# Kernel tuning notes

Measured on AMD Instinct MI355X. Metric: run time of the kernel, lower is better.

## Reference

```python
import jax, jax.numpy as jnp
import numpy as np

HIDDEN = 1024
HEADS = 16
D_K = HIDDEN // HEADS
NEG_INF = -jnp.inf


def setup_inputs() -> dict:
    key = jax.random.key(0)
    ks = jax.random.split(key, 9)
    N, S = 4, 2048
    scale = 1.0 / np.sqrt(HIDDEN)
    x = jax.random.normal(ks[0], (N, S, HIDDEN), dtype=jnp.float32)
    attn_mask = jnp.ones((N, S), dtype=jnp.int32)
    Wq = jax.random.normal(ks[1], (HIDDEN, HIDDEN), dtype=jnp.float32) * scale
    bq = jnp.zeros((HIDDEN,), dtype=jnp.float32)
    Wk = jax.random.normal(ks[2], (HIDDEN, HIDDEN), dtype=jnp.float32) * scale
    bk = jnp.zeros((HIDDEN,), dtype=jnp.float32)
    Wv = jax.random.normal(ks[3], (HIDDEN, HIDDEN), dtype=jnp.float32) * scale
    bv = jnp.zeros((HIDDEN,), dtype=jnp.float32)
    Wp = jax.random.normal(ks[4], (HIDDEN, HIDDEN), dtype=jnp.float32) * scale
    bp = jnp.zeros((HIDDEN,), dtype=jnp.float32)
    return {"x": x, "attn_mask": attn_mask, "Wq": Wq, "bq": bq,
            "Wk": Wk, "bk": bk, "Wv": Wv, "bv": bv, "Wp": Wp, "bp": bp}


def reference(x, attn_mask, Wq, bq, Wk, bk, Wv, bv, Wp, bp):
    N, S, _ = x.shape
    H, dk = HEADS, D_K
    # torch nn.Linear: y = x @ W.T + b
    q = (x @ Wq.T + bq).reshape(N, S, H, dk).transpose(0, 2, 1, 3)  # (N,H,S,dk)
    k = (x @ Wk.T + bk).reshape(N, S, H, dk).transpose(0, 2, 1, 3)
    v = (x @ Wv.T + bv).reshape(N, S, H, dk).transpose(0, 2, 1, 3)
    attn = jnp.einsum('nhqd,nhkd->nhqk', q, k) / jnp.sqrt(jnp.float32(dk))
    mask = attn_mask.reshape(N, 1, 1, S)
    attn = jnp.where(mask == 0, NEG_INF, attn)
    attn = jax.nn.softmax(attn, axis=-1)
    # dropout is identity in eval mode
    y = jnp.einsum('nhqk,nhkd->nhqd', attn, v)  # (N,H,S,dk)
    y = y.transpose(0, 2, 1, 3).reshape(N, S, H * dk)
    return y @ Wp.T + bp
```

## Files before the change

kernel.cpp:

```cpp
#include <hip/hip_runtime.h>

typedef unsigned short u16;
typedef unsigned int u32;
typedef unsigned long long u64;
typedef __attribute__((ext_vector_type(8))) short bf16x8;
typedef __attribute__((ext_vector_type(4))) short bf16x4;
typedef __attribute__((ext_vector_type(4))) float f32x4;
typedef __attribute__((ext_vector_type(2))) unsigned int u32x2;

#define AS1(p) ((const __attribute__((address_space(1))) void*)(p))
#define AS3(p) ((__attribute__((address_space(3))) void*)(p))

__device__ __forceinline__ u16 f2bf(float f) {
    u32 u = __float_as_uint(f);
    u += 0x7fff + ((u >> 16) & 1);
    return (u16)(u >> 16);
}
__device__ __forceinline__ u32 pack2bf(float lo, float hi) {
    u32 a = __float_as_uint(lo) + 0x8000u;
    u32 b = __float_as_uint(hi) + 0x8000u;
    return __builtin_amdgcn_perm(b, a, 0x07060302);
}
__device__ __forceinline__ u32 cvtpk(float lo, float hi) {
    u32 r;
    asm("v_cvt_pk_bf16_f32 %0, %1, %2" : "=v"(r) : "v"(lo), "v"(hi));
    return r;
}

__device__ __forceinline__ void async16(const u16* g, u16* l) {
    __builtin_amdgcn_global_load_lds(AS1(g), AS3(l), 16, 0, 0);
}

__global__ __launch_bounds__(256) void cvt_kernel(const float* __restrict__ src,
                                                  u16* __restrict__ dst, int n) {
    int idx = (blockIdx.x * 256 + threadIdx.x) * 8;
    if (idx >= n) return;
    float4 a = *(const float4*)(src + idx);
    float4 b = *(const float4*)(src + idx + 4);
    uint4 o;
    o.x = (u32)f2bf(a.x) | ((u32)f2bf(a.y) << 16);
    o.y = (u32)f2bf(a.z) | ((u32)f2bf(a.w) << 16);
    o.z = (u32)f2bf(b.x) | ((u32)f2bf(b.y) << 16);
    o.w = (u32)f2bf(b.z) | ((u32)f2bf(b.w) << 16);
    *(uint4*)(dst + idx) = o;
}

__global__ __launch_bounds__(256) void cvt4_kernel(
    const float* __restrict__ s0, const float* __restrict__ s1,
    const float* __restrict__ s2, const float* __restrict__ s3,
    u16* __restrict__ d0, u16* __restrict__ d1,
    u16* __restrict__ d2, u16* __restrict__ d3) {
    const float* s; u16* d;
    switch (blockIdx.y) {
        case 0:  s = s0; d = d0; break;
        case 1:  s = s1; d = d1; break;
        case 2:  s = s2; d = d2; break;
        default: s = s3; d = d3; break;
    }
    int idx = (blockIdx.x * 256 + threadIdx.x) * 8;
    float4 a = *(const float4*)(s + idx);
    float4 b = *(const float4*)(s + idx + 4);
    uint4 o;
    o.x = (u32)f2bf(a.x) | ((u32)f2bf(a.y) << 16);
    o.y = (u32)f2bf(a.z) | ((u32)f2bf(a.w) << 16);
    o.z = (u32)f2bf(b.x) | ((u32)f2bf(b.y) << 16);
    o.w = (u32)f2bf(b.z) | ((u32)f2bf(b.w) << 16);
    *(uint4*)(d + idx) = o;
}

__global__ __launch_bounds__(256, 2) void gemm_bt(
    const u16* __restrict__ A,
    const u16* __restrict__ Wa, const u16* __restrict__ Wb, const u16* __restrict__ Wc,
    const float* __restrict__ ba, const float* __restrict__ bb, const float* __restrict__ bc,
    void* oa, void* ob_, void* oc, int mode)
{
    constexpr int K = 1024;
    __shared__ u16 smem[128 * 132];

    const int tid = threadIdx.x;
    const int lane = tid & 63, wv = tid >> 6;
    const int l15 = lane & 15, quad = lane >> 4;
    const int wr = wv >> 1, wc = wv & 1;

    const int L = blockIdx.x + (blockIdx.y << 3) + (blockIdx.z << 9);
    const int g = L & 7;
    const int j = L >> 3;
    const int z = j >> 6;
    const int r = j & 63;
    const int m0 = ((g << 3) + (r & 7)) * 128;
    const int n0 = (r >> 3) * 128;

    const u16* W = (z == 0) ? Wa : ((z == 1) ? Wb : Wc);
    const float* bs = (z == 0) ? ba : ((z == 1) ? bb : bc);
    void* out = (z == 0) ? oa : ((z == 1) ? ob_ : oc);
    const bool swap_ = (mode == 1) || (z < 2);

    f32x4 acc[4][4];
#pragma unroll
    for (int i = 0; i < 4; ++i)
#pragma unroll
        for (int j2 = 0; j2 < 4; ++j2) acc[i][j2] = (f32x4)0.f;

    const int c0 = (wv * 2) * 64 + lane;
    const int c1 = c0 + 64;
    const int row0 = c0 >> 2, row1 = c1 >> 2;
    const int ko0 = ((c0 & 3) ^ (row0 & 3)) * 8;
    const int ko1 = ((c1 & 3) ^ (row1 & 3)) * 8;
    const u16* As0 = A + (size_t)(m0 + row0) * K + ko0;
    const u16* As1 = A + (size_t)(m0 + row1) * K + ko1;
    const u16* Ws0 = W + (size_t)(n0 + row0) * K + ko0;
    const u16* Ws1 = W + (size_t)(n0 + row1) * K + ko1;
    const int off0 = c0 * 8, off1 = c1 * 8;

    u16* const At0 = smem;         u16* const Wt0 = smem + 4096;
    u16* const At1 = smem + 8192;  u16* const Wt1 = smem + 12288;

    auto stage = [&](u16* Atb, u16* Wtb, int kk) {
        async16(As0 + kk, Atb + off0);
        async16(As1 + kk, Atb + off1);
        async16(Ws0 + kk, Wtb + off0);
        async16(Ws1 + kk, Wtb + off1);
    };
    auto compute = [&](const u16* Atb, const u16* Wtb) {
        bf16x8 af[4], wf[4];
#pragma unroll
        for (int t = 0; t < 4; ++t) {
            int rowa = wr * 64 + t * 16 + l15;
            af[t] = *(const bf16x8*)&Atb[rowa * 32 + ((quad ^ (rowa & 3)) * 8)];
            int rowb = wc * 64 + t * 16 + l15;
            wf[t] = *(const bf16x8*)&Wtb[rowb * 32 + ((quad ^ (rowb & 3)) * 8)];
        }
        if (swap_) {
#pragma unroll
            for (int rt = 0; rt < 4; ++rt)
#pragma unroll
                for (int ct = 0; ct < 4; ++ct)
                    acc[rt][ct] = __builtin_amdgcn_mfma_f32_16x16x32_bf16(wf[ct], af[rt], acc[rt][ct], 0, 0, 0);
        } else {
#pragma unroll
            for (int rt = 0; rt < 4; ++rt)
#pragma unroll
                for (int ct = 0; ct < 4; ++ct)
                    acc[rt][ct] = __builtin_amdgcn_mfma_f32_16x16x32_bf16(af[rt], wf[ct], acc[rt][ct], 0, 0, 0);
        }
    };

    stage(At0, Wt0, 0);
    asm volatile("s_waitcnt vmcnt(0)" ::: "memory");
    __builtin_amdgcn_s_barrier();

#pragma unroll 1
    for (int kk = 0; kk < K - 64; kk += 64) {
        stage(At1, Wt1, kk + 32);
        compute(At0, Wt0);
        asm volatile("s_waitcnt vmcnt(0)" ::: "memory");
        __builtin_amdgcn_s_barrier();
        stage(At0, Wt0, kk + 64);
        compute(At1, Wt1);
        asm volatile("s_waitcnt vmcnt(0)" ::: "memory");
        __builtin_amdgcn_s_barrier();
    }
    stage(At1, Wt1, 992);
    compute(At0, Wt0);
    asm volatile("s_waitcnt vmcnt(0)" ::: "memory");
    __builtin_amdgcn_s_barrier();
    compute(At1, Wt1);

    if (mode == 1) {
#pragma unroll
        for (int rt = 0; rt < 4; ++rt)
#pragma unroll
            for (int ct = 0; ct < 4; ++ct) {
                int m_ = m0 + wr * 64 + rt * 16 + l15;
                int ob = n0 + wc * 64 + ct * 16 + quad * 4;
                float4 b4 = *(const float4*)&bs[ob];
                float4 v;
                v.x = acc[rt][ct][0] + b4.x;
                v.y = acc[rt][ct][1] + b4.y;
                v.z = acc[rt][ct][2] + b4.z;
                v.w = acc[rt][ct][3] + b4.w;
                *(float4*)((float*)out + (size_t)m_ * 1024 + ob) = v;
            }
        return;
    }

    __syncthreads();

    const int n = m0 >> 11, s0 = m0 & 2047;
    if (z < 2) {
        const float qs = (z == 0) ? 0.18033688011112042f : 1.0f;
#pragma unroll
        for (int rt = 0; rt < 4; ++rt)
#pragma unroll
            for (int ct = 0; ct < 4; ++ct) {
                int ml = wr * 64 + rt * 16 + l15;
                int ol = wc * 64 + ct * 16 + quad * 4;
                float4 b4 = *(const float4*)&bs[n0 + ol];
                float v0 = (acc[rt][ct][0] + b4.x) * qs;
                float v1 = (acc[rt][ct][1] + b4.y) * qs;
                float v2 = (acc[rt][ct][2] + b4.z) * qs;
                float v3 = (acc[rt][ct][3] + b4.w) * qs;
                u32x2 pv = { pack2bf(v0, v1), pack2bf(v2, v3) };
                *(u32x2*)&smem[ml * 132 + ol] = pv;
            }
        __syncthreads();
        const int h0 = n0 >> 6;
#pragma unroll
        for (int p = 0; p < 8; ++p) {
            int hh = p >> 2, qq = p & 3;
            int m = qq * 32 + (tid >> 3), d = (tid & 7) * 8;
            bf16x8 vv = *(const bf16x8*)&smem[m * 132 + hh * 64 + d];
            u16* dst = (u16*)out + ((size_t)((n * 16 + h0 + hh) * 2048 + s0 + m)) * 64 + d;
            *(bf16x8*)dst = vv;
        }
    } else {
#pragma unroll
        for (int rt = 0; rt < 4; ++rt)
#pragma unroll
            for (int ct = 0; ct < 4; ++ct) {
                int ol = wc * 64 + ct * 16 + l15;
                int ml = wr * 64 + rt * 16 + quad * 4;
                float b = bs[n0 + ol];
                float v0 = acc[rt][ct][0] + b;
                float v1 = acc[rt][ct][1] + b;
                float v2 = acc[rt][ct][2] + b;
                float v3 = acc[rt][ct][3] + b;
                u32x2 pv = { pack2bf(v0, v1), pack2bf(v2, v3) };
                *(u32x2*)&smem[ol * 132 + ml] = pv;
            }
        __syncthreads();
#pragma unroll
        for (int p = 0; p < 8; ++p) {
            int o = p * 16 + (tid >> 4), ms = (tid & 15) * 8;
            bf16x8 vv = *(const bf16x8*)&smem[o * 132 + ms];
            int og = n0 + o;
            int h = og >> 6, d = og & 63;
            u16* dst = (u16*)out + ((size_t)((n * 16 + h) * 64 + d)) * 2048 + s0 + ms;
            *(bf16x8*)dst = vv;
        }
    }
}

__global__ __launch_bounds__(256, 2) void attn_kernel(
    const u16* __restrict__ Q, const u16* __restrict__ K_,
    const u16* __restrict__ VT, const int* __restrict__ mask,
    u16* __restrict__ Y)
{
    constexpr int S = 2048, DK = 64, STR = 72;
    __shared__ u16 Kt[2][64 * STR];
    __shared__ u16 Vt[2][64 * STR];

    const int tid = threadIdx.x;
    const int lane = tid & 63, w = tid >> 6;
    const int l15 = lane & 15, quad = lane >> 4;

    const int L = blockIdx.x + (blockIdx.y << 3);
    const int vb = (L & 7) * 64 + (L >> 3);
    const int nh = vb >> 3;
    const int n = nh >> 4, h = nh & 15;
    const int qbase = (vb & 7) * 256;

    const u16* Qh = Q + (size_t)nh * S * DK;
    const u16* Kh = K_ + (size_t)nh * S * DK;
    const u16* Vh = VT + (size_t)nh * DK * S;

    bf16x8 qf[4][2];
#pragma unroll
    for (int nt = 0; nt < 4; ++nt)
#pragma unroll
        for (int st = 0; st < 2; ++st)
            qf[nt][st] = *(const bf16x8*)(Qh + (size_t)(qbase + w * 64 + nt * 16 + l15) * DK + st * 32 + quad * 8);

    f32x4 o[4][4];
#pragma unroll
    for (int dt = 0; dt < 4; ++dt)
#pragma unroll
        for (int nt = 0; nt < 4; ++nt) o[dt][nt] = (f32x4)0.f;
    float lsum[4] = {0.f, 0.f, 0.f, 0.f};

    const int r0 = tid >> 3, c8 = (tid & 7) * 8;

    u32 bm = 0;
    for (int t = 0; t < 32; ++t) {
        int mv = mask[n * S + t * 64 + lane];
        if (__ballot(mv != 0) == ~0ull) bm |= (1u << t);
    }

    {
        bf16x8 k0 = *(const bf16x8*)(Kh + (size_t)r0 * 64 + c8);
        bf16x8 k1 = *(const bf16x8*)(Kh + (size_t)(r0 + 32) * 64 + c8);
        bf16x8 v0 = *(const bf16x8*)(Vh + (size_t)r0 * S + c8);
        bf16x8 v1 = *(const bf16x8*)(Vh + (size_t)(r0 + 32) * S + c8);
        *(bf16x8*)&Kt[0][r0 * STR + c8] = k0;
        *(bf16x8*)&Kt[0][(r0 + 32) * STR + c8] = k1;
        *(bf16x8*)&Vt[0][r0 * STR + c8] = v0;
        *(bf16x8*)&Vt[0][(r0 + 32) * STR + c8] = v1;
    }
    __syncthreads();

    const f32x4 zf = (f32x4)0.f;

    for (int it = 0; it < 32; ++it) {
        const int cur = it & 1, nxt = cur ^ 1;
        const u16* Ktc = &Kt[cur][0];
        const u16* Vtc = &Vt[cur][0];

        const int kkn = ((it + 1) << 6) & (S - 1);
        bf16x8 rk0 = *(const bf16x8*)(Kh + (size_t)(kkn + r0) * 64 + c8);
        bf16x8 rk1 = *(const bf16x8*)(Kh + (size_t)(kkn + r0 + 32) * 64 + c8);
        bf16x8 rv0 = *(const bf16x8*)(Vh + (size_t)r0 * S + kkn + c8);
        bf16x8 rv1 = *(const bf16x8*)(Vh + (size_t)(r0 + 32) * S + kkn + c8);

        f32x4 sacc[4][4];
        __builtin_amdgcn_s_setprio(1);
#pragma unroll
        for (int jt = 0; jt < 4; ++jt) {
            bf16x8 kf = *(const bf16x8*)&Ktc[(jt * 16 + l15) * STR + quad * 8];
#pragma unroll
            for (int nt = 0; nt < 4; ++nt)
                sacc[jt][nt] = __builtin_amdgcn_mfma_f32_16x16x32_bf16(kf, qf[nt][0], zf, 0, 0, 0);
        }
#pragma unroll
        for (int jt = 0; jt < 4; ++jt) {
            bf16x8 kf = *(const bf16x8*)&Ktc[(jt * 16 + l15) * STR + 32 + quad * 8];
#pragma unroll
            for (int nt = 0; nt < 4; ++nt)
                sacc[jt][nt] = __builtin_amdgcn_mfma_f32_16x16x32_bf16(kf, qf[nt][1], sacc[jt][nt], 0, 0, 0);
        }
        __builtin_amdgcn_s_setprio(0);

        if (!((bm >> it) & 1)) {
#pragma unroll
            for (int jt = 0; jt < 4; ++jt)
#pragma unroll
                for (int r = 0; r < 4; ++r) {
                    int mv = mask[n * S + it * 64 + jt * 16 + quad * 4 + r];
#pragma unroll
                    for (int nt = 0; nt < 4; ++nt)
                        if (mv == 0) sacc[jt][nt][r] = -1e30f;
                }
        }

        bf16x8 pb[4][2];
#pragma unroll
        for (int nt = 0; nt < 4; ++nt) {
            float ps = 0.f;
            u32 pkx[4], pky[4];
#pragma unroll
            for (int jt = 0; jt < 4; ++jt) {
                float e0 = __builtin_amdgcn_exp2f(sacc[jt][nt][0]);
                float e1 = __builtin_amdgcn_exp2f(sacc[jt][nt][1]);
                float e2 = __builtin_amdgcn_exp2f(sacc[jt][nt][2]);
                float e3 = __builtin_amdgcn_exp2f(sacc[jt][nt][3]);
                ps += (e0 + e1) + (e2 + e3);
                pkx[jt] = cvtpk(e0, e1);
                pky[jt] = cvtpk(e2, e3);
            }
            lsum[nt] += ps;
#pragma unroll
            for (int kt = 0; kt < 2; ++kt) {
                auto rX = __builtin_amdgcn_permlane32_swap(pkx[2 * kt], pkx[2 * kt + 1], false, false);
                auto rY = __builtin_amdgcn_permlane32_swap(pky[2 * kt], pky[2 * kt + 1], false, false);
                auto sX = __builtin_amdgcn_permlane16_swap(rX[0], rX[1], false, false);
                auto sY = __builtin_amdgcn_permlane16_swap(rY[0], rY[1], false, false);
                union { u32 u[4]; bf16x8 v; } pu;
                pu.u[0] = sX[0];
                pu.u[1] = sY[0];
                pu.u[2] = sX[1];
                pu.u[3] = sY[1];
                pb[nt][kt] = pu.v;
            }
        }

        *(bf16x8*)&Kt[nxt][r0 * STR + c8] = rk0;
        *(bf16x8*)&Kt[nxt][(r0 + 32) * STR + c8] = rk1;
        *(bf16x8*)&Vt[nxt][r0 * STR + c8] = rv0;
        *(bf16x8*)&Vt[nxt][(r0 + 32) * STR + c8] = rv1;

        __builtin_amdgcn_s_setprio(1);
#pragma unroll
        for (int kt = 0; kt < 2; ++kt) {
#pragma unroll
            for (int dt = 0; dt < 4; ++dt) {
                bf16x8 vf = *(const bf16x8*)&Vtc[(dt * 16 + l15) * STR + kt * 32 + quad * 8];
#pragma unroll
                for (int nt = 0; nt < 4; ++nt)
                    o[dt][nt] = __builtin_amdgcn_mfma_f32_16x16x32_bf16(vf, pb[nt][kt], o[dt][nt], 0, 0, 0);
            }
        }
        __builtin_amdgcn_s_setprio(0);

        __syncthreads();
    }

#pragma unroll
    for (int nt = 0; nt < 4; ++nt) {
        float ls = lsum[nt];
        ls += __shfl_xor(ls, 16);
        ls += __shfl_xor(ls, 32);
        float rl = (ls > 0.f) ? 1.f / ls : 0.f;
        int qi = qbase + w * 64 + nt * 16 + l15;
#pragma unroll
        for (int dt = 0; dt < 4; ++dt) {
            u32x2 pv = { pack2bf(o[dt][nt][0] * rl, o[dt][nt][1] * rl),
                         pack2bf(o[dt][nt][2] * rl, o[dt][nt][3] * rl) };
            size_t base = ((size_t)(n * 2048 + qi)) * 1024 + h * 64 + dt * 16 + quad * 4;
            *(u32x2*)(Y + base) = pv;
        }
    }
}

extern "C" void kernel_launch(void* const* d_in, const int* in_sizes, int n_in,
                              void* d_out, int out_size, void* d_ws, size_t ws_size,
                              hipStream_t stream) {
    const float* x  = (const float*)d_in[0];
    const int* mask = (const int*)d_in[1];
    const float* Wq = (const float*)d_in[2];
    const float* bq = (const float*)d_in[3];
    const float* Wk = (const float*)d_in[4];
    const float* bk = (const float*)d_in[5];
    const float* Wv = (const float*)d_in[6];
    const float* bv = (const float*)d_in[7];
    const float* Wp = (const float*)d_in[8];
    const float* bp = (const float*)d_in[9];

    char* ws = (char*)d_ws;
    u16* xb  = (u16*)(ws);
    u16* wqb = (u16*)(ws + (16u << 20));
    u16* wkb = (u16*)(ws + (18u << 20));
    u16* wvb = (u16*)(ws + (20u << 20));
    u16* wpb = (u16*)(ws + (22u << 20));
    u16* Qb  = (u16*)(ws + (24u << 20));
    u16* Kb  = (u16*)(ws + (40u << 20));
    u16* Vb  = (u16*)(ws + (56u << 20));
    u16* Yb  = (u16*)(ws + (72u << 20));

    cvt_kernel<<<4096, 256, 0, stream>>>(x, xb, 8388608);
    cvt4_kernel<<<dim3(512, 4), 256, 0, stream>>>(Wq, Wk, Wv, Wp, wqb, wkb, wvb, wpb);

    gemm_bt<<<dim3(8, 64, 3), 256, 0, stream>>>(xb, wqb, wkb, wvb, bq, bk, bv,
                                                (void*)Qb, (void*)Kb, (void*)Vb, 0);

    attn_kernel<<<dim3(8, 64), 256, 0, stream>>>(Qb, Kb, Vb, mask, Yb);

    gemm_bt<<<dim3(8, 64, 1), 256, 0, stream>>>(Yb, wpb, wpb, wpb, bp, bp, bp,
                                                d_out, d_out, d_out, 1);
}
```

Baseline: 268.7 us.

## Split QKV GEMM into dedicated kernel with 256x128 tiles and MFMA priority

Adds a dedicated QKV projection kernel whose block tile grows from 128x128 to 256x128. Each wave now computes 128x64 outputs, which raises reuse of the W fragments and halves the block count. The epilogue writes to shared memory in two passes. Both GEMMs raise wave priority around the MFMA loop with s_setprio, and the output projection becomes a specialised kernel without runtime mode branches. The trade-offs are higher register pressure (32 accumulator tiles per wave), 48KB of shared memory per block that may limit occupancy, and fewer blocks to spread across CUs.

```diff
diff --git a/kernel.cpp b/kernel.cpp
--- a/kernel.cpp
+++ b/kernel.cpp
@@ -68,32 +68,202 @@
     *(uint4*)(d + idx) = o;
 }
 
-__global__ __launch_bounds__(256, 2) void gemm_bt(
+__global__ __launch_bounds__(256, 2) void gemm_qkv(
     const u16* __restrict__ A,
     const u16* __restrict__ Wa, const u16* __restrict__ Wb, const u16* __restrict__ Wc,
     const float* __restrict__ ba, const float* __restrict__ bb, const float* __restrict__ bc,
-    void* oa, void* ob_, void* oc, int mode)
+    void* oa, void* ob_, void* oc)
 {
     constexpr int K = 1024;
-    __shared__ u16 smem[128 * 132];
+    __shared__ u16 smem[24576];
+
+    const int tid = threadIdx.x;
+    const int lane = tid & 63, wv = tid >> 6;
+    const int l15 = lane & 15, quad = lane >> 4;
+    const int wm = wv >> 1, wn = wv & 1;
+
+    const int L = blockIdx.x + (blockIdx.y << 3) + (blockIdx.z << 8);
+    const int g = L & 7;
+    const int j = L >> 3;
+    const int z = j >> 5;
+    const int r = j & 31;
+    const int m0 = ((g << 2) + (r & 3)) * 256;
+    const int n0 = (r >> 2) * 128;
+
+    const u16* W = (z == 0) ? Wa : ((z == 1) ? Wb : Wc);
+    const float* bs = (z == 0) ? ba : ((z == 1) ? bb : bc);
+    void* out = (z == 0) ? oa : ((z == 1) ? ob_ : oc);
+
+    f32x4 acc[8][4];
+#pragma unroll
+    for (int i = 0; i < 8; ++i)
+#pragma unroll
+        for (int j2 = 0; j2 < 4; ++j2) acc[i][j2] = (f32x4)0.f;
+
+    const u16* AsP[4]; int offA[4];
+#pragma unroll
+    for (int aj = 0; aj < 4; ++aj) {
+        int c = (wv * 4 + aj) * 64 + lane;
+        int row = c >> 2;
+        int ko = ((c & 3) ^ (row & 3)) * 8;
+        AsP[aj] = A + (size_t)(m0 + row) * K + ko;
+        offA[aj] = c * 8;
+    }
+    const u16* WsP[2]; int offW[2];
+#pragma unroll
+    for (int bj = 0; bj < 2; ++bj) {
+        int c = (wv * 2 + bj) * 64 + lane;
+        int row = c >> 2;
+        int ko = ((c & 3) ^ (row & 3)) * 8;
+        WsP[bj] = W + (size_t)(n0 + row) * K + ko;
+        offW[bj] = c * 8;
+    }
+
+    auto stage = [&](int buf, int kk) {
+        u16* At = smem + buf * 12288;
+        u16* Wt = At + 8192;
+#pragma unroll
+        for (int aj = 0; aj < 4; ++aj) async16(AsP[aj] + kk, At + offA[aj]);
+#pragma unroll
+        for (int bj = 0; bj < 2; ++bj) async16(WsP[bj] + kk, Wt + offW[bj]);
+    };
+    auto compute = [&](int buf) {
+        const u16* At = smem + buf * 12288;
+        const u16* Wt = At + 8192;
+        bf16x8 af[8], wf[4];
+#pragma unroll
+        for (int t = 0; t < 8; ++t) {
+            int rowa = wm * 128 + t * 16 + l15;
+            af[t] = *(const bf16x8*)&At[rowa * 32 + ((quad ^ (rowa & 3)) * 8)];
+        }
+#pragma unroll
+        for (int t = 0; t < 4; ++t) {
+            int rowb = wn * 64 + t * 16 + l15;
+            wf[t] = *(const bf16x8*)&Wt[rowb * 32 + ((quad ^ (rowb & 3)) * 8)];
+        }
+        __builtin_amdgcn_s_setprio(1);
+        if (z < 2) {
+#pragma unroll
+            for (int rt = 0; rt < 8; ++rt)
+#pragma unroll
+                for (int ct = 0; ct < 4; ++ct)
+                    acc[rt][ct] = __builtin_amdgcn_mfma_f32_16x16x32_bf16(wf[ct], af[rt], acc[rt][ct], 0, 0, 0);
+        } else {
+#pragma unroll
+            for (int rt = 0; rt < 8; ++rt)
+#pragma unroll
+                for (int ct = 0; ct < 4; ++ct)
+                    acc[rt][ct] = __builtin_amdgcn_mfma_f32_16x16x32_bf16(af[rt], wf[ct], acc[rt][ct], 0, 0, 0);
+        }
+        __builtin_amdgcn_s_setprio(0);
+    };
+
+    stage(0, 0);
+    asm volatile("s_waitcnt vmcnt(0)" ::: "memory");
+    __builtin_amdgcn_s_barrier();
+#pragma unroll 1
+    for (int kk = 0; kk < K - 64; kk += 64) {
+        stage(1, kk + 32);
+        compute(0);
+        asm volatile("s_waitcnt vmcnt(0)" ::: "memory");
+        __builtin_amdgcn_s_barrier();
+        stage(0, kk + 64);
+        compute(1);
+        asm volatile("s_waitcnt vmcnt(0)" ::: "memory");
+        __builtin_amdgcn_s_barrier();
+    }
+    stage(1, 992);
+    compute(0);
+    asm volatile("s_waitcnt vmcnt(0)" ::: "memory");
+    __builtin_amdgcn_s_barrier();
+    compute(1);
+
+    __syncthreads();
+
+    const int n = m0 >> 11, s0 = m0 & 2047;
+    const int h0 = n0 >> 6;
+    if (z < 2) {
+        const float qs = (z == 0) ? 0.18033688011112042f : 1.0f;
+#pragma unroll 1
+        for (int hp = 0; hp < 2; ++hp) {
+            if (wm == hp) {
+#pragma unroll
+                for (int rt = 0; rt < 8; ++rt)
+#pragma unroll
+                    for (int ct = 0; ct < 4; ++ct) {
+                        int ml = rt * 16 + l15;
+                        int ol = wn * 64 + ct * 16 + quad * 4;
+                        float4 b4 = *(const float4*)&bs[n0 + ol];
+                        float v0 = (acc[rt][ct][0] + b4.x) * qs;
+                        float v1 = (acc[rt][ct][1] + b4.y) * qs;
+                        float v2 = (acc[rt][ct][2] + b4.z) * qs;
+                        float v3 = (acc[rt][ct][3] + b4.w) * qs;
+                        u32x2 pv = { pack2bf(v0, v1), pack2bf(v2, v3) };
+                        *(u32x2*)&smem[ml * 132 + ol] = pv;
+                    }
+            }
+            __syncthreads();
+#pragma unroll
+            for (int p = 0; p < 8; ++p) {
+                int hh = p >> 2, qq = p & 3;
+                int m = qq * 32 + (tid >> 3), d = (tid & 7) * 8;
+                bf16x8 vv = *(const bf16x8*)&smem[m * 132 + hh * 64 + d];
+                u16* dst = (u16*)out + ((size_t)((n * 16 + h0 + hh) * 2048 + s0 + hp * 128 + m)) * 64 + d;
+                *(bf16x8*)dst = vv;
+            }
+            __syncthreads();
+        }
+    } else {
+#pragma unroll 1
+        for (int hp = 0; hp < 2; ++hp) {
+            if (wm == hp) {
+#pragma unroll
+                for (int rt = 0; rt < 8; ++rt)
+#pragma unroll
+                    for (int ct = 0; ct < 4; ++ct) {
+                        int ol = wn * 64 + ct * 16 + l15;
+                        int ml = rt * 16 + quad * 4;
+                        float b = bs[n0 + ol];
+                        float v0 = acc[rt][ct][0] + b;
+                        float v1 = acc[rt][ct][1] + b;
+                        float v2 = acc[rt][ct][2] + b;
+                        float v3 = acc[rt][ct][3] + b;
+                        u32x2 pv = { pack2bf(v0, v1), pack2bf(v2, v3) };
+                        *(u32x2*)&smem[ol * 132 + ml] = pv;
+                    }
+            }
+            __syncthreads();
+#pragma unroll
+            for (int p = 0; p < 8; ++p) {
+                int o = p * 16 + (tid >> 4), ms = (tid & 15) * 8;
+                bf16x8 vv = *(const bf16x8*)&smem[o * 132 + ms];
+                int og = n0 + o;
+                int h = og >> 6, d = og & 63;
+                u16* dst = (u16*)out + ((size_t)((n * 16 + h) * 64 + d)) * 2048 + s0 + hp * 128 + ms;
+                *(bf16x8*)dst = vv;
+            }
+            __syncthreads();
+        }
+    }
+}
+
+__global__ __launch_bounds__(256, 2) void gemm_bt(
+    const u16* __restrict__ A, const u16* __restrict__ Wa,
+    const float* __restrict__ ba, float* __restrict__ out)
+{
+    constexpr int K = 1024;
+    __shared__ u16 smem[16384];
 
     const int tid = threadIdx.x;
     const int lane = tid & 63, wv = tid >> 6;
     const int l15 = lane & 15, quad = lane >> 4;
     const int wr = wv >> 1, wc = wv & 1;
 
-    const int L = blockIdx.x + (blockIdx.y << 3) + (blockIdx.z << 9);
+    const int L = blockIdx.x + (blockIdx.y << 3);
     const int g = L & 7;
-    const int j = L >> 3;
-    const int z = j >> 6;
-    const int r = j & 63;
+    const int r = L >> 3;
     const int m0 = ((g << 3) + (r & 7)) * 128;
     const int n0 = (r >> 3) * 128;
-
-    const u16* W = (z == 0) ? Wa : ((z == 1) ? Wb : Wc);
-    const float* bs = (z == 0) ? ba : ((z == 1) ? bb : bc);
-    void* out = (z == 0) ? oa : ((z == 1) ? ob_ : oc);
-    const bool swap_ = (mode == 1) || (z < 2);
 
     f32x4 acc[4][4];
 #pragma unroll
@@ -108,8 +278,8 @@
     const int ko1 = ((c1 & 3) ^ (row1 & 3)) * 8;
     const u16* As0 = A + (size_t)(m0 + row0) * K + ko0;
     const u16* As1 = A + (size_t)(m0 + row1) * K + ko1;
-    const u16* Ws0 = W + (size_t)(n0 + row0) * K + ko0;
-    const u16* Ws1 = W + (size_t)(n0 + row1) * K + ko1;
+    const u16* Ws0 = Wa + (size_t)(n0 + row0) * K + ko0;
+    const u16* Ws1 = Wa + (size_t)(n0 + row1) * K + ko1;
     const int off0 = c0 * 8, off1 = c1 * 8;
 
     u16* const At0 = smem;         u16* const Wt0 = smem + 4096;
@@ -130,25 +300,18 @@
             int rowb = wc * 64 + t * 16 + l15;
             wf[t] = *(const bf16x8*)&Wtb[rowb * 32 + ((quad ^ (rowb & 3)) * 8)];
         }
-        if (swap_) {
-#pragma unroll
-            for (int rt = 0; rt < 4; ++rt)
-#pragma unroll
-                for (int ct = 0; ct < 4; ++ct)
-                    acc[rt][ct] = __builtin_amdgcn_mfma_f32_16x16x32_bf16(wf[ct], af[rt], acc[rt][ct], 0, 0, 0);
-        } else {
-#pragma unroll
-            for (int rt = 0; rt < 4; ++rt)
-#pragma unroll
-                for (int ct = 0; ct < 4; ++ct)
-                    acc[rt][ct] = __builtin_amdgcn_mfma_f32_16x16x32_bf16(af[rt], wf[ct], acc[rt][ct], 0, 0, 0);
-        }
+        __builtin_amdgcn_s_setprio(1);
+#pragma unroll
+        for (int rt = 0; rt < 4; ++rt)
+#pragma unroll
+            for (int ct = 0; ct < 4; ++ct)
+                acc[rt][ct] = __builtin_amdgcn_mfma_f32_16x16x32_bf16(wf[ct], af[rt], acc[rt][ct], 0, 0, 0);
+        __builtin_amdgcn_s_setprio(0);
     };
 
     stage(At0, Wt0, 0);
     asm volatile("s_waitcnt vmcnt(0)" ::: "memory");
     __builtin_amdgcn_s_barrier();
-
 #pragma unroll 1
     for (int kk = 0; kk < K - 64; kk += 64) {
         stage(At1, Wt1, kk + 32);
@@ -166,79 +329,20 @@
     __builtin_amdgcn_s_barrier();
     compute(At1, Wt1);
 
-    if (mode == 1) {
-#pragma unroll
-        for (int rt = 0; rt < 4; ++rt)
-#pragma unroll
-            for (int ct = 0; ct < 4; ++ct) {
-                int m_ = m0 + wr * 64 + rt * 16 + l15;
-                int ob = n0 + wc * 64 + ct * 16 + quad * 4;
-                float4 b4 = *(const float4*)&bs[ob];
-                float4 v;
-                v.x = acc[rt][ct][0] + b4.x;
-                v.y = acc[rt][ct][1] + b4.y;
-                v.z = acc[rt][ct][2] + b4.z;
-                v.w = acc[rt][ct][3] + b4.w;
-                *(float4*)((float*)out + (size_t)m_ * 1024 + ob) = v;
-            }
-        return;
-    }
-
-    __syncthreads();
-
-    const int n = m0 >> 11, s0 = m0 & 2047;
-    if (z < 2) {
-        const float qs = (z == 0) ? 0.18033688011112042f : 1.0f;
-#pragma unroll
-        for (int rt = 0; rt < 4; ++rt)
-#pragma unroll
-            for (int ct = 0; ct < 4; ++ct) {
-                int ml = wr * 64 + rt * 16 + l15;
-                int ol = wc * 64 + ct * 16 + quad * 4;
-                float4 b4 = *(const float4*)&bs[n0 + ol];
-                float v0 = (acc[rt][ct][0] + b4.x) * qs;
-                float v1 = (acc[rt][ct][1] + b4.y) * qs;
-                float v2 = (acc[rt][ct][2] + b4.z) * qs;
-                float v3 = (acc[rt][ct][3] + b4.w) * qs;
-                u32x2 pv = { pack2bf(v0, v1), pack2bf(v2, v3) };
-                *(u32x2*)&smem[ml * 132 + ol] = pv;
-            }
-        __syncthreads();
-        const int h0 = n0 >> 6;
-#pragma unroll
-        for (int p = 0; p < 8; ++p) {
-            int hh = p >> 2, qq = p & 3;
-            int m = qq * 32 + (tid >> 3), d = (tid & 7) * 8;
-            bf16x8 vv = *(const bf16x8*)&smem[m * 132 + hh * 64 + d];
-            u16* dst = (u16*)out + ((size_t)((n * 16 + h0 + hh) * 2048 + s0 + m)) * 64 + d;
-            *(bf16x8*)dst = vv;
-        }
-    } else {
-#pragma unroll
-        for (int rt = 0; rt < 4; ++rt)
-#pragma unroll
-            for (int ct = 0; ct < 4; ++ct) {
-                int ol = wc * 64 + ct * 16 + l15;
-                int ml = wr * 64 + rt * 16 + quad * 4;
-                float b = bs[n0 + ol];
-                float v0 = acc[rt][ct][0] + b;
-                float v1 = acc[rt][ct][1] + b;
-                float v2 = acc[rt][ct][2] + b;
-                float v3 = acc[rt][ct][3] + b;
-                u32x2 pv = { pack2bf(v0, v1), pack2bf(v2, v3) };
-                *(u32x2*)&smem[ol * 132 + ml] = pv;
-            }
-        __syncthreads();
-#pragma unroll
-        for (int p = 0; p < 8; ++p) {
-            int o = p * 16 + (tid >> 4), ms = (tid & 15) * 8;
-            bf16x8 vv = *(const bf16x8*)&smem[o * 132 + ms];
-            int og = n0 + o;
-            int h = og >> 6, d = og & 63;
-            u16* dst = (u16*)out + ((size_t)((n * 16 + h) * 64 + d)) * 2048 + s0 + ms;
-            *(bf16x8*)dst = vv;
-        }
-    }
+#pragma unroll
+    for (int rt = 0; rt < 4; ++rt)
+#pragma unroll
+        for (int ct = 0; ct < 4; ++ct) {
+            int m_ = m0 + wr * 64 + rt * 16 + l15;
+            int ob = n0 + wc * 64 + ct * 16 + quad * 4;
+            float4 b4 = *(const float4*)&ba[ob];
+            float4 v;
+            v.x = acc[rt][ct][0] + b4.x;
+            v.y = acc[rt][ct][1] + b4.y;
+            v.z = acc[rt][ct][2] + b4.z;
+            v.w = acc[rt][ct][3] + b4.w;
+            *(float4*)(out + (size_t)m_ * 1024 + ob) = v;
+        }
 }
 
 __global__ __launch_bounds__(256, 2) void attn_kernel(
@@ -438,11 +542,10 @@
     cvt_kernel<<<4096, 256, 0, stream>>>(x, xb, 8388608);
     cvt4_kernel<<<dim3(512, 4), 256, 0, stream>>>(Wq, Wk, Wv, Wp, wqb, wkb, wvb, wpb);
 
-    gemm_bt<<<dim3(8, 64, 3), 256, 0, stream>>>(xb, wqb, wkb, wvb, bq, bk, bv,
-                                                (void*)Qb, (void*)Kb, (void*)Vb, 0);
+    gemm_qkv<<<dim3(8, 32, 3), 256, 0, stream>>>(xb, wqb, wkb, wvb, bq, bk, bv,
+                                                 (void*)Qb, (void*)Kb, (void*)Vb);
 
     attn_kernel<<<dim3(8, 64), 256, 0, stream>>>(Qb, Kb, Vb, mask, Yb);
 
-    gemm_bt<<<dim3(8, 64, 1), 256, 0, stream>>>(Yb, wpb, wpb, wpb, bp, bp, bp,
-                                                d_out, d_out, d_out, 1);
-}
+    gemm_bt<<<dim3(8, 64), 256, 0, stream>>>(Yb, wpb, bp, (float*)d_out);
+}
```

New measurement: 630.0 us. 2.34x slower.
